# Optimization experiments

Hardware: AMD Instinct MI355X
Metric: run time of the kernel (lower is better)

## Reference

```python
import jax, jax.numpy as jnp
import numpy as np
import math

B, L, D, H, DK, DFF = 4, 1024, 1024, 16, 64, 4096
NUM_BUCKETS, MAX_DIST = 32, 128


def _relative_position_bucket(rel):
    # bidirectional T5 bucketing; rel = memory_pos - context_pos
    nb = NUM_BUCKETS // 2
    n = -rel
    ret = (n < 0).astype(jnp.int32) * nb
    n = jnp.abs(n)
    max_exact = nb // 2
    is_small = n < max_exact
    val_if_large = max_exact + (
        jnp.log(jnp.maximum(n, 1).astype(jnp.float32) / max_exact)
        / math.log(MAX_DIST / max_exact)
        * (nb - max_exact)
    ).astype(jnp.int32)
    val_if_large = jnp.minimum(val_if_large, nb - 1)
    return ret + jnp.where(is_small, n.astype(jnp.int32), val_if_large)


def t5_layernorm(x, w, eps):
    # no mean subtraction, no bias (T5 style)
    var = jnp.mean(jnp.square(x.astype(jnp.float32)), axis=-1, keepdims=True)
    return w * (x / jnp.sqrt(var + eps))


def setup_inputs() -> dict:
    key = jax.random.key(0)
    ks = jax.random.split(key, 12)
    inp = {
        "src": jax.random.normal(ks[0], (B, L, D), dtype=jnp.float32),
        "enc_position": jnp.broadcast_to(jnp.arange(L, dtype=jnp.int32), (B, L)),
        "ln1_w": jnp.ones((D,), jnp.float32),
        "wq": jax.random.normal(ks[1], (H * DK, D), jnp.float32) * (D * DK) ** -0.5,
        "bq": jnp.zeros((H * DK,), jnp.float32),
        "wk": jax.random.normal(ks[2], (H * DK, D), jnp.float32) * D ** -0.5,
        "bk": jnp.zeros((H * DK,), jnp.float32),
        "wv": jax.random.normal(ks[3], (H * DK, D), jnp.float32) * D ** -0.5,
        "bv": jnp.zeros((H * DK,), jnp.float32),
        "fc_w": jax.random.normal(ks[4], (D, H * DK), jnp.float32) * (H * DK) ** -0.5,
        "fc_b": jnp.zeros((D,), jnp.float32),
        "rel_bias": jax.random.normal(ks[5], (NUM_BUCKETS, H), jnp.float32) * 0.02,
        "ln2_w": jnp.ones((D,), jnp.float32),
        "wi": jax.random.normal(ks[6], (DFF, D), jnp.float32) * D ** -0.5,
        "wo": jax.random.normal(ks[7], (D, DFF), jnp.float32) * DFF ** -0.5,
    }
    return inp


def reference(src, enc_position, ln1_w, wq, bq, wk, bk, wv, bv, fc_w, fc_b,
              rel_bias, ln2_w, wi, wo):
    b, l, d = src.shape
    temp = DK ** 0.5

    # --- Multi-head self attention (pre-LN, T5 relative bias) ---
    proj = t5_layernorm(src, ln1_w, 1e-12)
    q = (proj @ wq.T + bq).reshape(b, l, H, DK).transpose(0, 2, 1, 3)  # [b,h,l,dk]
    k = (proj @ wk.T + bk).reshape(b, l, H, DK).transpose(0, 2, 1, 3)
    v = (proj @ wv.T + bv).reshape(b, l, H, DK).transpose(0, 2, 1, 3)

    # relative position bias: [b, h, l_q, l_k]
    rel = enc_position[:, None, :] - enc_position[:, :, None]  # mem - ctx
    bucket = _relative_position_bucket(rel)                    # [b, l, l]
    position_bias = rel_bias[bucket].transpose(0, 3, 1, 2)     # [b, h, l, l]

    scores = jnp.einsum("bhqd,bhkd->bhqk", q / temp, k) + position_bias
    attn = jax.nn.softmax(scores, axis=-1)                     # dropout = eval no-op
    ctx = jnp.einsum("bhqk,bhkd->bhqd", attn, v)
    ctx = ctx.transpose(0, 2, 1, 3).reshape(b, l, H * DK)
    attn_out = ctx @ fc_w.T + fc_b + src                       # residual
    attn_sum = jnp.sum(attn, axis=1)                           # [b, l, l]

    # --- Position-wise FFN (pre-LN, gelu, no biases) ---
    nx = t5_layernorm(attn_out, ln2_w, 1e-6)
    h = jax.nn.gelu(nx @ wi.T, approximate=False)
    out = attn_out + h @ wo.T
    return out, attn_sum, position_bias
```

## Files before the change

kernel.cpp:

```cpp
#include <hip/hip_runtime.h>
#include <hip/hip_bf16.h>
#include <math.h>

typedef __attribute__((ext_vector_type(8))) short short8;
typedef __attribute__((ext_vector_type(4))) float f32x4;
typedef unsigned short u16;

#define L2E 1.44269504088896340736f

__device__ __forceinline__ u16 f2bf(float f) {
  union { float f; unsigned u; } x; x.f = f;
  unsigned r = x.u + 0x7fffu + ((x.u >> 16) & 1u);
  return (u16)(r >> 16);
}

__device__ __forceinline__ void gload16(const void* g, void* l) {
  auto gp = reinterpret_cast<const __attribute__((address_space(1))) void*>(
      reinterpret_cast<uintptr_t>(g));
  auto lp = reinterpret_cast<__attribute__((address_space(3))) void*>(
      reinterpret_cast<uintptr_t>(l));
  __builtin_amdgcn_global_load_lds(gp, lp, 16, 0, 0);
}

__device__ __forceinline__ int bucket_fn(int rel) {
  int n = -rel;
  int ret = 0;
  if (n < 0) { ret = 16; n = -n; }
  if (n < 8) return ret + n;
  int e = 31 - __clz(n);
  unsigned nn = (unsigned)n * (unsigned)n;
  int f = 2 * e + ((nn >= (1u << (2 * e + 1))) ? 1 : 0) - 6;
  int val = 8 + f;
  if (val > 15) val = 15;
  return ret + val;
}

__global__ __launch_bounds__(256) void prep(
    const float* __restrict__ wq, const float* __restrict__ wk,
    const float* __restrict__ wv, const float* __restrict__ fcw,
    const float* __restrict__ wi, const float* __restrict__ wo,
    const float* __restrict__ bq, const float* __restrict__ bk,
    const float* __restrict__ bv, const float* __restrict__ rel_bias,
    u16* __restrict__ wqb, u16* __restrict__ wkb, u16* __restrict__ wvb,
    u16* __restrict__ fcwb, u16* __restrict__ wib, u16* __restrict__ wob,
    float* __restrict__ fb, float* __restrict__ tab) {
  const int blk = blockIdx.x, t = threadIdx.x;
  if (blk < 12288) {
    const float* s; u16* d; int rel;
    if (blk < 1024)      { s = wq;  d = wqb;  rel = blk; }
    else if (blk < 2048) { s = wk;  d = wkb;  rel = blk - 1024; }
    else if (blk < 3072) { s = wv;  d = wvb;  rel = blk - 2048; }
    else if (blk < 4096) { s = fcw; d = fcwb; rel = blk - 3072; }
    else if (blk < 8192) { s = wi;  d = wib;  rel = blk - 4096; }
    else                 { s = wo;  d = wob;  rel = blk - 8192; }
    const int i = (rel * 256 + t) * 4;
    float4 v = *(const float4*)&s[i];
    d[i + 0] = f2bf(v.x); d[i + 1] = f2bf(v.y);
    d[i + 2] = f2bf(v.z); d[i + 3] = f2bf(v.w);
  } else if (blk < 12300) {
    const int i = (blk - 12288) * 256 + t;
    fb[i] = i < 1024 ? bq[i] : (i < 2048 ? bk[i - 1024] : bv[i - 2048]);
  } else {
    const int idx = (blk - 12300) * 256 + t;
    const int h = idx >> 11;
    const int rel = (idx & 2047) - 1024;
    tab[idx] = rel_bias[bucket_fn(rel) * 16 + h];
  }
}

__global__ __launch_bounds__(256) void write_pb(const float* __restrict__ tab,
                                                float* __restrict__ pb) {
  const int i = blockIdx.x, h = blockIdx.y, t = threadIdx.x;
  __shared__ float tabs[2048];
  ((float4*)tabs)[t]       = ((const float4*)(tab + h * 2048))[t];
  ((float4*)tabs)[t + 256] = ((const float4*)(tab + h * 2048))[t + 256];
  __syncthreads();
  const int j = t * 4;
  float4 o;
  o.x = tabs[j + 0 - i + 1024];
  o.y = tabs[j + 1 - i + 1024];
  o.z = tabs[j + 2 - i + 1024];
  o.w = tabs[j + 3 - i + 1024];
#pragma unroll
  for (int b = 0; b < 4; b++)
    *(float4*)&pb[(((size_t)(b * 16 + h)) * 1024 + i) * 1024 + j] = o;
}

__global__ __launch_bounds__(256) void t5_ln(const float* __restrict__ x,
                                             const float* __restrict__ wgt,
                                             float eps, u16* __restrict__ out) {
  const int row = blockIdx.x, t = threadIdx.x;
  const float4 v = ((const float4*)(x + (size_t)row * 1024))[t];
  float ss = v.x * v.x + v.y * v.y + v.z * v.z + v.w * v.w;
#pragma unroll
  for (int off = 1; off < 64; off <<= 1) ss += __shfl_xor(ss, off, 64);
  __shared__ float red[4];
  if ((t & 63) == 0) red[t >> 6] = ss;
  __syncthreads();
  float tot = red[0] + red[1] + red[2] + red[3];
  float inv = 1.0f / sqrtf(tot * (1.0f / 1024.0f) + eps);
  const float4 wv = ((const float4*)wgt)[t];
  u16* o = out + (size_t)row * 1024 + t * 4;
  o[0] = f2bf(v.x * inv * wv.x);
  o[1] = f2bf(v.y * inv * wv.y);
  o[2] = f2bf(v.z * inv * wv.z);
  o[3] = f2bf(v.w * inv * wv.w);
}

__global__ __launch_bounds__(256) void transpose_v(const u16* __restrict__ v,
                                                   u16* __restrict__ vt) {
  __shared__ u16 T[64][72];
  const int bh = blockIdx.y;
  const int l0 = blockIdx.x * 64;
  const int t = threadIdx.x;
  const int sr = t >> 3, sc = (t & 7) * 8;
  const u16* vb = v + (size_t)bh * 65536;
  *(short8*)&T[sr][sc]      = *(const short8*)&vb[(size_t)(l0 + sr) * 64 + sc];
  *(short8*)&T[sr + 32][sc] = *(const short8*)&vb[(size_t)(l0 + sr + 32) * 64 + sc];
  __syncthreads();
  u16* vtb = vt + (size_t)bh * 65536;
  short8 o0, o1;
#pragma unroll
  for (int u = 0; u < 8; u++) {
    ((u16*)&o0)[u] = T[sc + u][sr];
    ((u16*)&o1)[u] = T[sc + u][sr + 32];
  }
  *(short8*)&vtb[(size_t)sr * 1024 + l0 + sc]        = o0;
  *(short8*)&vtb[(size_t)(sr + 32) * 1024 + l0 + sc] = o1;
}

template<int MODE>
__global__ __launch_bounds__(256, 3) void gemm_nt(
    const u16* __restrict__ A, const u16* __restrict__ Bw,
    int M, int N, int K,
    const float* __restrict__ bias, const float* __restrict__ res,
    float scale, float* __restrict__ outF, u16* __restrict__ outB) {
  __shared__ u16 As[3][4096];
  __shared__ u16 Bs[3][4096];
  const int t = threadIdx.x;
  const int w = t >> 6, lane = t & 63;
  const int wr = w >> 1, wc = w & 1;
  const int g = lane >> 4, lc = lane & 15;
  const int m0 = blockIdx.y * 128, n0 = blockIdx.x * 128;

  const int srow = w * 16 + (lane >> 2);
  const int sc8  = (lane & 3) ^ ((srow >> 1) & 3);
  const u16* Ag = &A[(size_t)(m0 + srow) * K + sc8 * 8];
  const u16* Bg = &Bw[(size_t)(n0 + srow) * K + sc8 * 8];
  const size_t row64 = (size_t)64 * K;
  const int swz = (lc >> 1) & 3;

  const int NT = K >> 5;
  f32x4 acc[4][4] = {};

  auto stage = [&](int buf, int tt) {
    const int k0 = tt << 5;
    u16* lA = &As[buf][w * 512];
    u16* lB = &Bs[buf][w * 512];
    gload16(Ag + k0, lA);
    gload16(Ag + row64 + k0, lA + 2048);
    gload16(Bg + k0, lB);
    gload16(Bg + row64 + k0, lB + 2048);
  };

  stage(0, 0);
  stage(1, 1);

  for (int tt = 0; tt < NT; tt++) {
    const int cur = tt % 3;
    if (tt < NT - 1) {
      asm volatile("s_waitcnt vmcnt(4)" ::: "memory");
    } else {
      asm volatile("s_waitcnt vmcnt(0)" ::: "memory");
    }
    __builtin_amdgcn_s_barrier();
    short8 af[4], bf[4];
#pragma unroll
    for (int mi = 0; mi < 4; mi++)
      af[mi] = *(short8*)&As[cur][(wr * 64 + mi * 16 + lc) * 32 + (g ^ swz) * 8];
#pragma unroll
    for (int ni = 0; ni < 4; ni++)
      bf[ni] = *(short8*)&Bs[cur][(wc * 64 + ni * 16 + lc) * 32 + (g ^ swz) * 8];
    if (tt + 2 < NT) stage((tt + 2) % 3, tt + 2);
#pragma unroll
    for (int mi = 0; mi < 4; mi++)
#pragma unroll
      for (int ni = 0; ni < 4; ni++)
        acc[mi][ni] = __builtin_amdgcn_mfma_f32_16x16x32_bf16(af[mi], bf[ni], acc[mi][ni], 0, 0, 0);
  }

  u16* Es = &As[0][0];
  __syncthreads();
#pragma unroll
  for (int mi = 0; mi < 4; mi++) {
#pragma unroll
    for (int ni = 0; ni < 4; ni++) {
#pragma unroll
      for (int r = 0; r < 4; r++) {
        const int col = n0 + wc * 64 + ni * 16 + lc;
        float v = acc[mi][ni][r];
        if (MODE == 0) {
          v = (v + bias[col]) * ((col >> 10) == 0 ? scale : 1.0f);
        } else {
          v = 0.5f * v * (1.0f + erff(v * 0.70710678118654752440f));
        }
        Es[wr * 2048 + (g * 4 + r) * 128 + wc * 64 + ni * 16 + lc] = f2bf(v);
      }
    }
    __syncthreads();
    {
      const int rr = t >> 3;
      const int wr2 = rr >> 4, r16 = rr & 15;
      const int cc = (t & 7) * 16;
      short8 o0 = *(short8*)&Es[wr2 * 2048 + r16 * 128 + cc];
      short8 o1 = *(short8*)&Es[wr2 * 2048 + r16 * 128 + cc + 8];
      const int row = m0 + wr2 * 64 + mi * 16 + r16;
      if (MODE == 0) {
        const int col0 = n0 + cc;
        const int which = col0 >> 10, c = col0 & 1023;
        const int hh = c >> 6, dk = c & 63;
        const int b = row >> 10, pos = row & 1023;
        u16* dst = outB + (size_t)which * 4194304 +
                   (((size_t)(b * 16 + hh)) * 1024 + pos) * 64 + dk;
        *(short8*)dst = o0;
        *(short8*)(dst + 8) = o1;
      } else {
        u16* dst = outB + (size_t)row * (size_t)N + n0 + cc;
        *(short8*)dst = o0;
        *(short8*)(dst + 8) = o1;
      }
    }
    __syncthreads();
  }
}

template<int MODE>
__global__ __launch_bounds__(256, 4) void gemm_nt64(
    const u16* __restrict__ A, const u16* __restrict__ Bw,
    int M, int N, int K,
    const float* __restrict__ bias, const float* __restrict__ res,
    float* __restrict__ outF) {
  __shared__ u16 As[3][2048];
  __shared__ u16 Bs[3][4096];
  const int t = threadIdx.x;
  const int w = t >> 6, lane = t & 63;
  const int wr = w >> 1, wc = w & 1;
  const int g = lane >> 4, lc = lane & 15;
  const int m0 = blockIdx.y * 64, n0 = blockIdx.x * 128;

  const int srow = w * 16 + (lane >> 2);
  const int sc8  = (lane & 3) ^ ((srow >> 1) & 3);
  const u16* Ag = &A[(size_t)(m0 + srow) * K + sc8 * 8];
  const u16* Bg = &Bw[(size_t)(n0 + srow) * K + sc8 * 8];
  const size_t row64 = (size_t)64 * K;
  const int swz = (lc >> 1) & 3;

  const int NT = K >> 5;
  f32x4 acc[2][4] = {};

  auto stage = [&](int buf, int tt) {
    const int k0 = tt << 5;
    gload16(Ag + k0, &As[buf][w * 512]);
    gload16(Bg + k0, &Bs[buf][w * 512]);
    gload16(Bg + row64 + k0, &Bs[buf][w * 512 + 2048]);
  };

  stage(0, 0);
  stage(1, 1);

  for (int tt = 0; tt < NT; tt++) {
    const int cur = tt % 3;
    if (tt < NT - 1) {
      asm volatile("s_waitcnt vmcnt(3)" ::: "memory");
    } else {
      asm volatile("s_waitcnt vmcnt(0)" ::: "memory");
    }
    __builtin_amdgcn_s_barrier();
    short8 af[2], bf[4];
#pragma unroll
    for (int mi = 0; mi < 2; mi++)
      af[mi] = *(short8*)&As[cur][(wr * 32 + mi * 16 + lc) * 32 + (g ^ swz) * 8];
#pragma unroll
    for (int ni = 0; ni < 4; ni++)
      bf[ni] = *(short8*)&Bs[cur][(wc * 64 + ni * 16 + lc) * 32 + (g ^ swz) * 8];
    if (tt + 2 < NT) stage((tt + 2) % 3, tt + 2);
#pragma unroll
    for (int mi = 0; mi < 2; mi++)
#pragma unroll
      for (int ni = 0; ni < 4; ni++)
        acc[mi][ni] = __builtin_amdgcn_mfma_f32_16x16x32_bf16(af[mi], bf[ni], acc[mi][ni], 0, 0, 0);
  }

#pragma unroll
  for (int mi = 0; mi < 2; mi++) {
#pragma unroll
    for (int ni = 0; ni < 4; ni++) {
#pragma unroll
      for (int r = 0; r < 4; r++) {
        const int row = m0 + wr * 32 + mi * 16 + g * 4 + r;
        const int col = n0 + wc * 64 + ni * 16 + lc;
        float v = acc[mi][ni][r];
        if (MODE == 1) {
          v += bias[col] + res[(size_t)row * 1024 + col];
        } else {
          v += res[(size_t)row * 1024 + col];
        }
        outF[(size_t)row * 1024 + col] = v;
      }
    }
  }
}

__global__ __launch_bounds__(256) void attn_kernel(
    const u16* __restrict__ q, const u16* __restrict__ k,
    const u16* __restrict__ vt, const float* __restrict__ tab,
    u16* __restrict__ ctx, float* __restrict__ ml) {
  const int bh = blockIdx.y;
  const int h = bh & 15, b = bh >> 4;
  const int i0 = blockIdx.x * 64;
  const int t = threadIdx.x, w = t >> 6, lane = t & 63;
  const int g = lane >> 4, lc = lane & 15;
  const int sr = t >> 3;
  const int swc = ((t & 7) ^ (sr & 7)) * 8;
  const int sc = (t & 7) * 8;

  __shared__ u16 Ks[2][64][64];
  __shared__ u16 Vts[2][64][64];
  __shared__ u16 P[4][16][64];
  __shared__ float tabs[2048];

  const u16* qb  = q + (size_t)bh * 65536;
  const u16* kb  = k + (size_t)bh * 65536;
  const u16* vtb = vt + (size_t)bh * 65536;

  {
    float4 t0 = ((const float4*)(tab + h * 2048))[t];
    float4 t1 = ((const float4*)(tab + h * 2048))[t + 256];
    t0.x *= L2E; t0.y *= L2E; t0.z *= L2E; t0.w *= L2E;
    t1.x *= L2E; t1.y *= L2E; t1.z *= L2E; t1.w *= L2E;
    ((float4*)tabs)[t]       = t0;
    ((float4*)tabs)[t + 256] = t1;
  }

  const short8 aq0 = *(const short8*)&qb[(size_t)(i0 + w * 16 + lc) * 64 + g * 8];
  const short8 aq1 = *(const short8*)&qb[(size_t)(i0 + w * 16 + lc) * 64 + 32 + g * 8];

  {
    short8 ka = *(const short8*)&kb[(size_t)sr * 64 + sc];
    short8 kc = *(const short8*)&kb[(size_t)(sr + 32) * 64 + sc];
    short8 va = *(const short8*)&vtb[(size_t)sr * 1024 + sc];
    short8 vc = *(const short8*)&vtb[(size_t)(sr + 32) * 1024 + sc];
    *(short8*)&Ks[0][sr][swc]       = ka;
    *(short8*)&Ks[0][sr + 32][swc]  = kc;
    *(short8*)&Vts[0][sr][swc]      = va;
    *(short8*)&Vts[0][sr + 32][swc] = vc;
  }
  __syncthreads();

  const int rx = lc & 7;
  const int ibase = 1024 - i0 - (w * 16 + g * 4) + lc;

  float m_r[4] = {-INFINITY, -INFINITY, -INFINITY, -INFINITY};
  float l_r[4] = {0.f, 0.f, 0.f, 0.f};
  f32x4 cacc[4] = {};

  for (int tt = 0; tt < 16; tt++) {
    const int buf = tt & 1;
    const int j0 = tt * 64;

    short8 nka, nkc, nva, nvc;
    if (tt < 15) {
      const int jn = j0 + 64;
      nka = *(const short8*)&kb[(size_t)(jn + sr) * 64 + sc];
      nkc = *(const short8*)&kb[(size_t)(jn + sr + 32) * 64 + sc];
      nva = *(const short8*)&vtb[(size_t)sr * 1024 + jn + sc];
      nvc = *(const short8*)&vtb[(size_t)(sr + 32) * 1024 + jn + sc];
    }

    f32x4 s[4] = {};
#pragma unroll
    for (int ni = 0; ni < 4; ni++) {
      short8 b0 = *(short8*)&Ks[buf][ni * 16 + lc][(g ^ rx) * 8];
      short8 b1 = *(short8*)&Ks[buf][ni * 16 + lc][((4 + g) ^ rx) * 8];
      s[ni] = __builtin_amdgcn_mfma_f32_16x16x32_bf16(aq0, b0, s[ni], 0, 0, 0);
      s[ni] = __builtin_amdgcn_mfma_f32_16x16x32_bf16(aq1, b1, s[ni], 0, 0, 0);
    }
#pragma unroll
    for (int ni = 0; ni < 4; ni++)
#pragma unroll
      for (int r = 0; r < 4; r++)
        s[ni][r] += tabs[ibase + j0 + ni * 16 - r];

#pragma unroll
    for (int r = 0; r < 4; r++) {
      float tm = fmaxf(fmaxf(s[0][r], s[1][r]), fmaxf(s[2][r], s[3][r]));
#pragma unroll
      for (int off = 1; off < 16; off <<= 1) tm = fmaxf(tm, __shfl_xor(tm, off, 64));
      const float mn = fmaxf(m_r[r], tm);
      const float scl = __builtin_amdgcn_exp2f(m_r[r] - mn);
      float rs = 0.f;
#pragma unroll
      for (int ni = 0; ni < 4; ni++) {
        float p = __builtin_amdgcn_exp2f(s[ni][r] - mn);
        s[ni][r] = p;
        rs += p;
      }
#pragma unroll
      for (int off = 1; off < 16; off <<= 1) rs += __shfl_xor(rs, off, 64);
      l_r[r] = l_r[r] * scl + rs;
      m_r[r] = mn;
#pragma unroll
      for (int d = 0; d < 4; d++) cacc[d][r] *= scl;
    }

#pragma unroll
    for (int ni = 0; ni < 4; ni++)
#pragma unroll
      for (int r = 0; r < 4; r++) {
        const int prow = g * 4 + r;
        P[w][prow][(((ni * 2 + (lc >> 3)) ^ (prow & 7)) << 3) | (lc & 7)] = f2bf(s[ni][r]);
      }

    short8 ap0 = *(short8*)&P[w][lc][(g ^ rx) * 8];
    short8 ap1 = *(short8*)&P[w][lc][((4 + g) ^ rx) * 8];
#pragma unroll
    for (int d = 0; d < 4; d++) {
      short8 bv0 = *(short8*)&Vts[buf][d * 16 + lc][(g ^ rx) * 8];
      short8 bv1 = *(short8*)&Vts[buf][d * 16 + lc][((4 + g) ^ rx) * 8];
      cacc[d] = __builtin_amdgcn_mfma_f32_16x16x32_bf16(ap0, bv0, cacc[d], 0, 0, 0);
      cacc[d] = __builtin_amdgcn_mfma_f32_16x16x32_bf16(ap1, bv1, cacc[d], 0, 0, 0);
    }

    if (tt < 15) {
      *(short8*)&Ks[buf ^ 1][sr][swc]       = nka;
      *(short8*)&Ks[buf ^ 1][sr + 32][swc]  = nkc;
      *(short8*)&Vts[buf ^ 1][sr][swc]      = nva;
      *(short8*)&Vts[buf ^ 1][sr + 32][swc] = nvc;
    }
    __syncthreads();
  }

  float inv[4];
#pragma unroll
  for (int r = 0; r < 4; r++) inv[r] = 1.0f / l_r[r];
#pragma unroll
  for (int d = 0; d < 4; d++)
#pragma unroll
    for (int r = 0; r < 4; r++) {
      const int pos = i0 + w * 16 + g * 4 + r;
      ctx[((size_t)b * 1024 + pos) * 1024 + h * 64 + d * 16 + lc] = f2bf(cacc[d][r] * inv[r]);
    }
  if (lc == 0) {
#pragma unroll
    for (int r = 0; r < 4; r++) {
      const int i = i0 + w * 16 + g * 4 + r;
      ml[(size_t)bh * 1024 + i] = m_r[r];
      ml[65536 + (size_t)bh * 1024 + i] = l_r[r];
    }
  }
}

__global__ __launch_bounds__(256) void attn_sum_kernel(
    const u16* __restrict__ q, const u16* __restrict__ k,
    const float* __restrict__ tab, const float* __restrict__ ml,
    float* __restrict__ asum) {
  const int b = blockIdx.z;
  const int i0 = blockIdx.y * 64;
  const int j0 = blockIdx.x * 64;
  const int t = threadIdx.x, w = t >> 6, lane = t & 63;
  const int g = lane >> 4, lc = lane & 15;
  const int sr = t >> 3;
  const int swc = ((t & 7) ^ (sr & 7)) * 8;
  const int sc = (t & 7) * 8;
  const int rx = lc & 7;
  __shared__ u16 Ks[64][64];
  __shared__ float tabs[128];

  f32x4 acc[4] = {};

  for (int h = 0; h < 16; h++) {
    const int bh = b * 16 + h;
    __syncthreads();
    const u16* kb = k + (size_t)bh * 65536;
    *(short8*)&Ks[sr][swc]      = *(const short8*)&kb[(size_t)(j0 + sr) * 64 + sc];
    *(short8*)&Ks[sr + 32][swc] = *(const short8*)&kb[(size_t)(j0 + sr + 32) * 64 + sc];
    if (t < 127) tabs[t] = tab[h * 2048 + (j0 - i0 - 63 + t) + 1024] * L2E;
    __syncthreads();
    const u16* qb = q + (size_t)bh * 65536;
    short8 aq0 = *(const short8*)&qb[(size_t)(i0 + w * 16 + lc) * 64 + g * 8];
    short8 aq1 = *(const short8*)&qb[(size_t)(i0 + w * 16 + lc) * 64 + 32 + g * 8];
    f32x4 s[4] = {};
#pragma unroll
    for (int ni = 0; ni < 4; ni++) {
      short8 b0 = *(short8*)&Ks[ni * 16 + lc][(g ^ rx) * 8];
      short8 b1 = *(short8*)&Ks[ni * 16 + lc][((4 + g) ^ rx) * 8];
      s[ni] = __builtin_amdgcn_mfma_f32_16x16x32_bf16(aq0, b0, s[ni], 0, 0, 0);
      s[ni] = __builtin_amdgcn_mfma_f32_16x16x32_bf16(aq1, b1, s[ni], 0, 0, 0);
    }
    float mm[4], li[4];
#pragma unroll
    for (int r = 0; r < 4; r++) {
      const int i = i0 + w * 16 + g * 4 + r;
      mm[r] = ml[(size_t)bh * 1024 + i];
      li[r] = 1.0f / ml[65536 + (size_t)bh * 1024 + i];
    }
#pragma unroll
    for (int ni = 0; ni < 4; ni++)
#pragma unroll
      for (int r = 0; r < 4; r++) {
        float sv = s[ni][r] + tabs[ni * 16 + lc - w * 16 - g * 4 - r + 63];
        acc[ni][r] += __builtin_amdgcn_exp2f(sv - mm[r]) * li[r];
      }
  }
#pragma unroll
  for (int ni = 0; ni < 4; ni++)
#pragma unroll
    for (int r = 0; r < 4; r++) {
      const int i = i0 + w * 16 + g * 4 + r;
      asum[((size_t)b * 1024 + i) * 1024 + j0 + ni * 16 + lc] = acc[ni][r];
    }
}

extern "C" void kernel_launch(void* const* d_in, const int* in_sizes, int n_in,
                              void* d_out, int out_size, void* d_ws, size_t ws_size,
                              hipStream_t stream) {
  const float* src      = (const float*)d_in[0];
  const float* ln1_w    = (const float*)d_in[2];
  const float* wq       = (const float*)d_in[3];
  const float* bq       = (const float*)d_in[4];
  const float* wk       = (const float*)d_in[5];
  const float* bk       = (const float*)d_in[6];
  const float* wv       = (const float*)d_in[7];
  const float* bv       = (const float*)d_in[8];
  const float* fc_w     = (const float*)d_in[9];
  const float* fc_b     = (const float*)d_in[10];
  const float* rel_bias = (const float*)d_in[11];
  const float* ln2_w    = (const float*)d_in[12];
  const float* wi       = (const float*)d_in[13];
  const float* wo       = (const float*)d_in[14];

  const size_t MB = 1u << 20;
  char* ws = (char*)d_ws;
  u16* wq_b   = (u16*)(ws + 0 * MB);
  u16* wk_b   = (u16*)(ws + 2 * MB);
  u16* wv_b   = (u16*)(ws + 4 * MB);
  u16* fcw_b  = (u16*)(ws + 6 * MB);
  u16* wi_b   = (u16*)(ws + 8 * MB);
  u16* wo_b   = (u16*)(ws + 16 * MB);
  u16* proj_b = (u16*)(ws + 24 * MB);
  u16* q_b    = (u16*)(ws + 32 * MB);
  u16* k_b    = (u16*)(ws + 40 * MB);
  u16* v_b    = (u16*)(ws + 48 * MB);
  u16* vt_b   = (u16*)(ws + 56 * MB);
  u16* h_b    = (u16*)(ws + 32 * MB);
  u16* ctx_b  = (u16*)(ws + 64 * MB);
  float* attn_out = (float*)(ws + 72 * MB);
  float* ml   = (float*)(ws + 88 * MB);
  float* tab  = (float*)(ws + 88 * MB + 512 * 1024);
  float* fb   = (float*)(ws + 90 * MB);

  float* outF = (float*)d_out;
  float* asum = outF + 4194304;
  float* pb   = outF + 8388608;

  prep<<<12428, 256, 0, stream>>>(wq, wk, wv, fc_w, wi, wo, bq, bk, bv, rel_bias,
                                  wq_b, wk_b, wv_b, fcw_b, wi_b, wo_b, fb, tab);

  write_pb<<<dim3(1024, 16), 256, 0, stream>>>(tab, pb);

  t5_ln<<<4096, 256, 0, stream>>>(src, ln1_w, 1e-12f, proj_b);

  gemm_nt<0><<<dim3(24, 32), 256, 0, stream>>>(proj_b, wq_b, 4096, 3072, 1024, fb, nullptr,
                                               0.125f * L2E, nullptr, q_b);

  transpose_v<<<dim3(16, 64), 256, 0, stream>>>(v_b, vt_b);
  attn_kernel<<<dim3(16, 64), 256, 0, stream>>>(q_b, k_b, vt_b, tab, ctx_b, ml);
  attn_sum_kernel<<<dim3(16, 16, 4), 256, 0, stream>>>(q_b, k_b, tab, ml, asum);

  gemm_nt64<1><<<dim3(8, 64), 256, 0, stream>>>(ctx_b, fcw_b, 4096, 1024, 1024, fc_b, src, attn_out);

  t5_ln<<<4096, 256, 0, stream>>>(attn_out, ln2_w, 1e-6f, proj_b);

  gemm_nt<2><<<dim3(32, 32), 256, 0, stream>>>(proj_b, wi_b, 4096, 4096, 1024, nullptr, nullptr, 1.0f, nullptr, h_b);
  gemm_nt64<3><<<dim3(8, 64), 256, 0, stream>>>(h_b, wo_b, 4096, 1024, 4096, nullptr, attn_out, outF);
}
```

Baseline: 366.3 us.

## Use 128x256 GEMM tiles for QKV/FFN-in and 128x128 for FFN-out, add setprio

Adds a new gemm_wide kernel with 128x256 output tiles (8 MFMA columns per wave) for the QKV projection and the FFN up-projection. The gemm_nt kernel is repurposed as a 128x128 fp32-residual-epilogue GEMM for the FFN down-projection, replacing the 64x128 kernel. s_setprio is raised around the MFMA loops in all GEMMs. Larger tiles raise arithmetic intensity and cut global traffic, at the cost of fewer blocks (384/512/256), lower occupancy and more register pressure.

```diff
diff --git a/kernel.cpp b/kernel.cpp
--- a/kernel.cpp
+++ b/kernel.cpp
@@ -130,11 +130,123 @@
 }
 
 template<int MODE>
+__global__ __launch_bounds__(256, 2) void gemm_wide(
+    const u16* __restrict__ A, const u16* __restrict__ Bw,
+    int M, int N, int K,
+    const float* __restrict__ bias, float scale, u16* __restrict__ outB) {
+  __shared__ u16 As[3][4096];
+  __shared__ u16 Bs[3][8192];
+  const int t = threadIdx.x;
+  const int w = t >> 6, lane = t & 63;
+  const int wr = w >> 1, wc = w & 1;
+  const int g = lane >> 4, lc = lane & 15;
+  const int m0 = blockIdx.y * 128, n0 = blockIdx.x * 256;
+
+  const int srowA = w * 32 + (lane >> 2);
+  const int srowB = w * 64 + (lane >> 2);
+  const int scA = (lane & 3) ^ ((srowA >> 1) & 3);
+  const int scB = (lane & 3) ^ ((srowB >> 1) & 3);
+  const u16* Ag = &A[(size_t)(m0 + srowA) * K + scA * 8];
+  const u16* Bg = &Bw[(size_t)(n0 + srowB) * K + scB * 8];
+  const size_t row16 = (size_t)16 * K;
+  const int swz = (lc >> 1) & 3;
+
+  const int NT = K >> 5;
+  f32x4 acc[4][8] = {};
+
+  auto stage = [&](int buf, int tt) {
+    const int k0 = tt << 5;
+    u16* lA = &As[buf][w * 1024];
+    u16* lB = &Bs[buf][w * 2048];
+    gload16(Ag + k0, lA);
+    gload16(Ag + row16 + k0, lA + 512);
+    gload16(Bg + k0, lB);
+    gload16(Bg + row16 + k0, lB + 512);
+    gload16(Bg + 2 * row16 + k0, lB + 1024);
+    gload16(Bg + 3 * row16 + k0, lB + 1536);
+  };
+
+  stage(0, 0);
+  stage(1, 1);
+
+  for (int tt = 0; tt < NT; tt++) {
+    const int cur = tt % 3;
+    if (tt < NT - 1) {
+      asm volatile("s_waitcnt vmcnt(6)" ::: "memory");
+    } else {
+      asm volatile("s_waitcnt vmcnt(0)" ::: "memory");
+    }
+    __builtin_amdgcn_s_barrier();
+    short8 af[4], bf[8];
+#pragma unroll
+    for (int mi = 0; mi < 4; mi++)
+      af[mi] = *(short8*)&As[cur][(wr * 64 + mi * 16 + lc) * 32 + (g ^ swz) * 8];
+#pragma unroll
+    for (int ni = 0; ni < 8; ni++)
+      bf[ni] = *(short8*)&Bs[cur][(wc * 128 + ni * 16 + lc) * 32 + (g ^ swz) * 8];
+    if (tt + 2 < NT) stage((tt + 2) % 3, tt + 2);
+    __builtin_amdgcn_s_setprio(1);
+#pragma unroll
+    for (int mi = 0; mi < 4; mi++)
+#pragma unroll
+      for (int ni = 0; ni < 8; ni++)
+        acc[mi][ni] = __builtin_amdgcn_mfma_f32_16x16x32_bf16(af[mi], bf[ni], acc[mi][ni], 0, 0, 0);
+    __builtin_amdgcn_s_setprio(0);
+  }
+
+  u16* Es = &As[0][0];
+  __syncthreads();
+#pragma unroll
+  for (int mi = 0; mi < 4; mi++) {
+#pragma unroll
+    for (int ni = 0; ni < 8; ni++) {
+#pragma unroll
+      for (int r = 0; r < 4; r++) {
+        const int col = n0 + wc * 128 + ni * 16 + lc;
+        float v = acc[mi][ni][r];
+        if (MODE == 0) {
+          v = (v + bias[col]) * ((col >> 10) == 0 ? scale : 1.0f);
+        } else {
+          v = 0.5f * v * (1.0f + erff(v * 0.70710678118654752440f));
+        }
+        Es[(wr * 16 + g * 4 + r) * 256 + wc * 128 + ni * 16 + lc] = f2bf(v);
+      }
+    }
+    __syncthreads();
+    {
+      const int r16 = t >> 4;
+      const int cc = (t & 15) * 16;
+#pragma unroll
+      for (int wr2 = 0; wr2 < 2; wr2++) {
+        short8 o0 = *(short8*)&Es[(wr2 * 16 + r16) * 256 + cc];
+        short8 o1 = *(short8*)&Es[(wr2 * 16 + r16) * 256 + cc + 8];
+        const int row = m0 + wr2 * 64 + mi * 16 + r16;
+        if (MODE == 0) {
+          const int col0 = n0 + cc;
+          const int which = col0 >> 10, c = col0 & 1023;
+          const int hh = c >> 6, dk = c & 63;
+          const int b = row >> 10, pos = row & 1023;
+          u16* dst = outB + (size_t)which * 4194304 +
+                     (((size_t)(b * 16 + hh)) * 1024 + pos) * 64 + dk;
+          *(short8*)dst = o0;
+          *(short8*)(dst + 8) = o1;
+        } else {
+          u16* dst = outB + (size_t)row * (size_t)N + n0 + cc;
+          *(short8*)dst = o0;
+          *(short8*)(dst + 8) = o1;
+        }
+      }
+    }
+    __syncthreads();
+  }
+}
+
+template<int MODE>
 __global__ __launch_bounds__(256, 3) void gemm_nt(
     const u16* __restrict__ A, const u16* __restrict__ Bw,
     int M, int N, int K,
     const float* __restrict__ bias, const float* __restrict__ res,
-    float scale, float* __restrict__ outF, u16* __restrict__ outB) {
+    float* __restrict__ outF) {
   __shared__ u16 As[3][4096];
   __shared__ u16 Bs[3][4096];
   const int t = threadIdx.x;
@@ -182,55 +294,32 @@
     for (int ni = 0; ni < 4; ni++)
       bf[ni] = *(short8*)&Bs[cur][(wc * 64 + ni * 16 + lc) * 32 + (g ^ swz) * 8];
     if (tt + 2 < NT) stage((tt + 2) % 3, tt + 2);
+    __builtin_amdgcn_s_setprio(1);
 #pragma unroll
     for (int mi = 0; mi < 4; mi++)
 #pragma unroll
       for (int ni = 0; ni < 4; ni++)
         acc[mi][ni] = __builtin_amdgcn_mfma_f32_16x16x32_bf16(af[mi], bf[ni], acc[mi][ni], 0, 0, 0);
-  }
-
-  u16* Es = &As[0][0];
-  __syncthreads();
+    __builtin_amdgcn_s_setprio(0);
+  }
+
 #pragma unroll
   for (int mi = 0; mi < 4; mi++) {
 #pragma unroll
     for (int ni = 0; ni < 4; ni++) {
 #pragma unroll
       for (int r = 0; r < 4; r++) {
+        const int row = m0 + wr * 64 + mi * 16 + g * 4 + r;
         const int col = n0 + wc * 64 + ni * 16 + lc;
         float v = acc[mi][ni][r];
-        if (MODE == 0) {
-          v = (v + bias[col]) * ((col >> 10) == 0 ? scale : 1.0f);
+        if (MODE == 1) {
+          v += bias[col] + res[(size_t)row * 1024 + col];
         } else {
-          v = 0.5f * v * (1.0f + erff(v * 0.70710678118654752440f));
+          v += res[(size_t)row * 1024 + col];
         }
-        Es[wr * 2048 + (g * 4 + r) * 128 + wc * 64 + ni * 16 + lc] = f2bf(v);
+        outF[(size_t)row * 1024 + col] = v;
       }
     }
-    __syncthreads();
-    {
-      const int rr = t >> 3;
-      const int wr2 = rr >> 4, r16 = rr & 15;
-      const int cc = (t & 7) * 16;
-      short8 o0 = *(short8*)&Es[wr2 * 2048 + r16 * 128 + cc];
-      short8 o1 = *(short8*)&Es[wr2 * 2048 + r16 * 128 + cc + 8];
-      const int row = m0 + wr2 * 64 + mi * 16 + r16;
-      if (MODE == 0) {
-        const int col0 = n0 + cc;
-        const int which = col0 >> 10, c = col0 & 1023;
-        const int hh = c >> 6, dk = c & 63;
-        const int b = row >> 10, pos = row & 1023;
-        u16* dst = outB + (size_t)which * 4194304 +
-                   (((size_t)(b * 16 + hh)) * 1024 + pos) * 64 + dk;
-        *(short8*)dst = o0;
-        *(short8*)(dst + 8) = o1;
-      } else {
-        u16* dst = outB + (size_t)row * (size_t)N + n0 + cc;
-        *(short8*)dst = o0;
-        *(short8*)(dst + 8) = o1;
-      }
-    }
-    __syncthreads();
   }
 }
 
@@ -284,11 +373,13 @@
     for (int ni = 0; ni < 4; ni++)
       bf[ni] = *(short8*)&Bs[cur][(wc * 64 + ni * 16 + lc) * 32 + (g ^ swz) * 8];
     if (tt + 2 < NT) stage((tt + 2) % 3, tt + 2);
+    __builtin_amdgcn_s_setprio(1);
 #pragma unroll
     for (int mi = 0; mi < 2; mi++)
 #pragma unroll
       for (int ni = 0; ni < 4; ni++)
         acc[mi][ni] = __builtin_amdgcn_mfma_f32_16x16x32_bf16(af[mi], bf[ni], acc[mi][ni], 0, 0, 0);
+    __builtin_amdgcn_s_setprio(0);
   }
 
 #pragma unroll
@@ -570,8 +661,8 @@
 
   t5_ln<<<4096, 256, 0, stream>>>(src, ln1_w, 1e-12f, proj_b);
 
-  gemm_nt<0><<<dim3(24, 32), 256, 0, stream>>>(proj_b, wq_b, 4096, 3072, 1024, fb, nullptr,
-                                               0.125f * L2E, nullptr, q_b);
+  gemm_wide<0><<<dim3(12, 32), 256, 0, stream>>>(proj_b, wq_b, 4096, 3072, 1024,
+                                                 fb, 0.125f * L2E, q_b);
 
   transpose_v<<<dim3(16, 64), 256, 0, stream>>>(v_b, vt_b);
   attn_kernel<<<dim3(16, 64), 256, 0, stream>>>(q_b, k_b, vt_b, tab, ctx_b, ml);
@@ -581,6 +672,8 @@
 
   t5_ln<<<4096, 256, 0, stream>>>(attn_out, ln2_w, 1e-6f, proj_b);
 
-  gemm_nt<2><<<dim3(32, 32), 256, 0, stream>>>(proj_b, wi_b, 4096, 4096, 1024, nullptr, nullptr, 1.0f, nullptr, h_b);
-  gemm_nt64<3><<<dim3(8, 64), 256, 0, stream>>>(h_b, wo_b, 4096, 1024, 4096, nullptr, attn_out, outF);
-}
+  gemm_wide<2><<<dim3(16, 32), 256, 0, stream>>>(proj_b, wi_b, 4096, 4096, 1024,
+                                                 nullptr, 1.0f, h_b);
+  gemm_nt<3><<<dim3(8, 32), 256, 0, stream>>>(h_b, wo_b, 4096, 1024, 4096,
+                                              nullptr, attn_out, outF);
+}
```

Result: slower. 382.9 us (+4.6%).
